# Kernel tuning notes

Measured on AMD Instinct MI355X. Metric: run time of the kernel, lower is better.

The kernel has to match this reference:

```python
import jax, jax.numpy as jnp
import numpy as np

N, E, D, H = 50000, 500000, 128, 4
FH = D // H  # per-head dim of gat1
NEG_SLOPE = 0.2
EPS = 1e-16  # PyG softmax denominator epsilon


def _gat_layer(x, src, dst, W, a_src, a_dst, bias, heads, fh):
    # W: [D_in, heads*fh]; a_src/a_dst: [heads, fh]; bias: [heads*fh]
    n = x.shape[0]
    xp = (x @ W).reshape(n, heads, fh)                     # [N,H,F]
    alpha_s = jnp.einsum('nhf,hf->nh', xp, a_src)          # [N,H]
    alpha_d = jnp.einsum('nhf,hf->nh', xp, a_dst)
    e = alpha_s[src] + alpha_d[dst]                        # [E,H]
    e = jnp.where(e > 0, e, NEG_SLOPE * e)                 # leaky_relu
    # edge softmax grouped by destination node
    m = jax.lax.stop_gradient(jax.ops.segment_max(e, dst, num_segments=n))
    a = jnp.exp(e - m[dst])
    denom = jax.ops.segment_sum(a, dst, num_segments=n)
    a = a / (denom[dst] + EPS)                             # [E,H]
    msg = a[:, :, None] * xp[src]                          # [E,H,F]
    out = jax.ops.segment_sum(msg, dst, num_segments=n)    # [N,H,F]
    return out.reshape(n, heads * fh) + bias


def setup_inputs() -> dict:
    key = jax.random.key(0)
    ks = jax.random.split(key, 20)

    def glorot(k, shape):
        fan_in, fan_out = shape[0], shape[-1]
        std = (2.0 / (fan_in + fan_out)) ** 0.5
        return std * jax.random.normal(k, shape, dtype=jnp.float32)

    inp = {
        'x': jax.random.normal(ks[0], (N, 1), dtype=jnp.float32),
        'edge_index': jax.random.randint(ks[1], (E, 2), 0, N, dtype=jnp.int64 if jax.config.jax_enable_x64 else jnp.int32),
        'W_emb': glorot(ks[2], (1, D)),   # nn.Linear(1, d_node), stored as [in,out]
        'b_emb': jnp.zeros((D,), jnp.float32),
        # gat1: in=D, heads=H, per-head out=FH
        'W1': glorot(ks[3], (D, H * FH)),
        'as1': glorot(ks[4], (H, FH)),
        'ad1': glorot(ks[5], (H, FH)),
        'b1': jnp.zeros((H * FH,), jnp.float32),
        # gat2/3/4: in=D, heads=1, out=D
        'W2': glorot(ks[6], (D, D)), 'as2': glorot(ks[7], (1, D)), 'ad2': glorot(ks[8], (1, D)), 'b2': jnp.zeros((D,), jnp.float32),
        'W3': glorot(ks[9], (D, D)), 'as3': glorot(ks[10], (1, D)), 'ad3': glorot(ks[11], (1, D)), 'b3': jnp.zeros((D,), jnp.float32),
        'W4': glorot(ks[12], (D, D)), 'as4': glorot(ks[13], (1, D)), 'ad4': glorot(ks[14], (1, D)), 'b4': jnp.zeros((D,), jnp.float32),
    }
    return inp


def reference(x, edge_index, W_emb, b_emb, W1, as1, ad1, b1,
              W2, as2, ad2, b2, W3, as3, ad3, b3, W4, as4, ad4, b4):
    # emb: Linear(1 -> D)
    h = x @ W_emb + b_emb                                  # [N,D]
    # edge_index.t(): row 0 = src, row 1 = dst; GATConv adds self-loops
    loop = jnp.arange(N, dtype=edge_index.dtype)
    src = jnp.concatenate([edge_index[:, 0], loop])
    dst = jnp.concatenate([edge_index[:, 1], loop])
    h = jax.nn.relu(_gat_layer(h, src, dst, W1, as1, ad1, b1, H, FH))
    h = jax.nn.relu(_gat_layer(h, src, dst, W2, as2, ad2, b2, 1, D))
    h = jax.nn.relu(_gat_layer(h, src, dst, W3, as3, ad3, b3, 1, D))
    h = _gat_layer(h, src, dst, W4, as4, ad4, b4, 1, D)
    return h
```

## Files before the change

### kernel.cpp

```cpp
#include <hip/hip_runtime.h>
#include <math.h>


#define LEAKY(e) ((e) > 0.f ? (e) : 0.2f * (e))
#define SCAN_BLK 1024

typedef __attribute__((ext_vector_type(8))) short bf16x8;
typedef __attribute__((ext_vector_type(4))) float f32x4;

__device__ inline ushort f32_to_bf16_rne(float f) {
    unsigned u = __float_as_uint(f);
    unsigned r = (u + 0x7FFFu + ((u >> 16) & 1u)) >> 16;
    return (ushort)r;
}
__device__ inline float bf16_to_f32(ushort h) { return __uint_as_float((unsigned)h << 16); }
__device__ inline unsigned pack2(float a, float b) {
    return (unsigned)f32_to_bf16_rne(a) | ((unsigned)f32_to_bf16_rne(b) << 16);
}


__global__ void k_hist(const int* __restrict__ ei, int E, int N, int* __restrict__ deg) {
    int e = blockIdx.x * blockDim.x + threadIdx.x;
    int Et = E + N;
    if (e >= Et) return;
    int dst = (e < E) ? ei[2 * e + 1] : (e - E);
    atomicAdd(&deg[dst], 1);
}

__global__ __launch_bounds__(SCAN_BLK) void k_scan1(const int* __restrict__ deg,
                                                    int* __restrict__ tmp,
                                                    int* __restrict__ blocksum, int n) {
    __shared__ int buf[SCAN_BLK];
    int tid = threadIdx.x;
    int gid = blockIdx.x * SCAN_BLK + tid;
    int v = (gid < n) ? deg[gid] : 0;
    buf[tid] = v;
    __syncthreads();
#pragma unroll
    for (int off = 1; off < SCAN_BLK; off <<= 1) {
        int t = (tid >= off) ? buf[tid - off] : 0;
        __syncthreads();
        buf[tid] += t;
        __syncthreads();
    }
    if (gid < n) tmp[gid] = buf[tid] - v;
    if (tid == SCAN_BLK - 1) blocksum[blockIdx.x] = buf[tid];
}

__global__ __launch_bounds__(256) void k_scan2(const int* __restrict__ blocksum,
                                               int* __restrict__ blockoff, int nb,
                                               int* __restrict__ row_ptr, int n) {
    __shared__ int buf[256];
    int tid = threadIdx.x;
    int v = (tid < nb) ? blocksum[tid] : 0;
    buf[tid] = v;
    __syncthreads();
#pragma unroll
    for (int off = 1; off < 256; off <<= 1) {
        int t = (tid >= off) ? buf[tid - off] : 0;
        __syncthreads();
        buf[tid] += t;
        __syncthreads();
    }
    if (tid < nb) blockoff[tid] = buf[tid] - v;
    if (tid == 255) row_ptr[n] = buf[tid];
}

__global__ void k_scan3(const int* __restrict__ tmp, const int* __restrict__ blockoff,
                        int* __restrict__ row_ptr, int* __restrict__ cursor, int n) {
    int gid = blockIdx.x * blockDim.x + threadIdx.x;
    if (gid >= n) return;
    int v = tmp[gid] + blockoff[gid / SCAN_BLK];
    row_ptr[gid] = v;
    cursor[gid] = v;
}

__global__ void k_scatter(const int* __restrict__ ei, int E, int N,
                          int* __restrict__ cursor, int* __restrict__ csr_src) {
    int e = blockIdx.x * blockDim.x + threadIdx.x;
    int Et = E + N;
    if (e >= Et) return;
    int src, dst;
    if (e < E) { src = ei[2 * e]; dst = ei[2 * e + 1]; }
    else { src = dst = e - E; }
    int pos = atomicAdd(&cursor[dst], 1);
    csr_src[pos] = src;
}


__global__ void k_wsplit3(const float* __restrict__ W0, const float* __restrict__ W1,
                          const float* __restrict__ W2,
                          ushort* __restrict__ hi0, ushort* __restrict__ lo0,
                          ushort* __restrict__ hi1, ushort* __restrict__ lo1,
                          ushort* __restrict__ hi2, ushort* __restrict__ lo2) {
    int l = blockIdx.x >> 6;
    int idx = (blockIdx.x & 63) * 256 + threadIdx.x;
    const float* W = (l == 0) ? W0 : (l == 1) ? W1 : W2;
    ushort* ph = (l == 0) ? hi0 : (l == 1) ? hi1 : hi2;
    ushort* pl = (l == 0) ? lo0 : (l == 1) ? lo1 : lo2;
    int k = idx >> 7, c = idx & 127;
    float w = W[idx];
    ushort hi = f32_to_bf16_rne(w);
    ushort lo = f32_to_bf16_rne(w - bf16_to_f32(hi));
    ph[c * 128 + k] = hi;
    pl[c * 128 + k] = lo;
}

__global__ void k_wvec3(const float* __restrict__ W0, const float* __restrict__ W1,
                        const float* __restrict__ W2,
                        const float* __restrict__ as0, const float* __restrict__ as1,
                        const float* __restrict__ as2,
                        const float* __restrict__ ad0, const float* __restrict__ ad1,
                        const float* __restrict__ ad2,
                        float* __restrict__ was0, float* __restrict__ was1,
                        float* __restrict__ was2,
                        float* __restrict__ wad0, float* __restrict__ wad1,
                        float* __restrict__ wad2) {
    int l = blockIdx.x;
    const float* W  = (l == 0) ? W0 : (l == 1) ? W1 : W2;
    const float* av = (l == 0) ? as0 : (l == 1) ? as1 : as2;
    const float* dv = (l == 0) ? ad0 : (l == 1) ? ad1 : ad2;
    float* ws = (l == 0) ? was0 : (l == 1) ? was1 : was2;
    float* wd = (l == 0) ? wad0 : (l == 1) ? wad1 : wad2;
    int k = threadIdx.x;
    float s = 0.f, d = 0.f;
    for (int c = 0; c < 128; c++) {
        float w = W[k * 128 + c];
        s += w * av[c];
        d += w * dv[c];
    }
    ws[k] = s; wd[k] = d;
}


__global__ void k_emb(const float* __restrict__ W_emb, const float* __restrict__ b_emb,
                      const float* __restrict__ W1, const float* __restrict__ as1,
                      const float* __restrict__ ad1, float* __restrict__ consts) {
    __shared__ float su[128], sv[128];
    int f = threadIdx.x;
    float u = 0.f, v = 0.f;
    for (int k = 0; k < 128; k++) {
        u += W_emb[k] * W1[k * 128 + f];
        v += b_emb[k] * W1[k * 128 + f];
    }
    su[f] = u; sv[f] = v;
    consts[f] = u; consts[128 + f] = v;
    __syncthreads();
    if (f < 4) {
        float P = 0.f, Q = 0.f, R = 0.f, S = 0.f;
        for (int j = 0; j < 32; j++) {
            float uu = su[f * 32 + j], vv = sv[f * 32 + j];
            float a = as1[f * 32 + j], d = ad1[f * 32 + j];
            P += uu * a; Q += vv * a; R += uu * d; S += vv * d;
        }
        consts[256 + f] = P; consts[260 + f] = Q; consts[264 + f] = R; consts[268 + f] = S;
    }
}

__global__ __launch_bounds__(256) void k_l1(const float* __restrict__ x,
        const int* __restrict__ row_ptr, const int* __restrict__ csr_src,
        const float* __restrict__ consts, const float* __restrict__ b1,
        const float* __restrict__ was2, const float* __restrict__ wad2,
        float* __restrict__ hout, float* __restrict__ a_s, float* __restrict__ a_d, int n) {
    __shared__ float sm[64][4], smw[64][4];
    int tid = threadIdx.x;
    int nl = tid >> 2, q = tid & 3;
    int node = blockIdx.x * 64 + nl;
    bool valid = node < n;
    float P = consts[256 + q], Q = consts[260 + q];
    float R = consts[264 + q], Sc = consts[268 + q];
    float den = 0.f, S = 0.f;
    if (valid) {
        float xd = x[node];
        float c0 = xd * R + Sc + Q;
        int s0 = row_ptr[node], s1 = row_ptr[node + 1];
        for (int i = s0; i < s1; i++) {
            float xs = x[csr_src[i]];
            float e = xs * P + c0;
            e = LEAKY(e);
            float w = __expf(e);
            den += w;
            S += w * xs;
        }
    }
    float inv = 1.f / (den + 1e-16f);
    sm[nl][q] = S * inv;
    smw[nl][q] = den * inv;
    __syncthreads();
    float Sn = sm[nl][q], Swn = smw[nl][q];
    float ps = 0.f, pd = 0.f;
    if (valid) {
#pragma unroll
        for (int j = 0; j < 8; j++) {
            int f = q * 32 + j * 4;
            float4 u = *(const float4*)(consts + f);
            float4 v = *(const float4*)(consts + 128 + f);
            float4 b = *(const float4*)(b1 + f);
            float4 ws = *(const float4*)(was2 + f);
            float4 wd = *(const float4*)(wad2 + f);
            float4 val;
            val.x = fmaxf(Sn * u.x + Swn * v.x + b.x, 0.f);
            val.y = fmaxf(Sn * u.y + Swn * v.y + b.y, 0.f);
            val.z = fmaxf(Sn * u.z + Swn * v.z + b.z, 0.f);
            val.w = fmaxf(Sn * u.w + Swn * v.w + b.w, 0.f);
            *(float4*)(hout + (size_t)node * 128 + f) = val;
            ps += val.x * ws.x + val.y * ws.y + val.z * ws.z + val.w * ws.w;
            pd += val.x * wd.x + val.y * wd.y + val.z * wd.z + val.w * wd.w;
        }
    }
    ps += __shfl_xor(ps, 1, 64); ps += __shfl_xor(ps, 2, 64);
    pd += __shfl_xor(pd, 1, 64); pd += __shfl_xor(pd, 2, 64);
    if (q == 0 && valid) { a_s[node] = ps; a_d[node] = pd; }
}

__global__ __launch_bounds__(256) void k_aggh(const float* __restrict__ h,
        const float* __restrict__ as, const float* __restrict__ ad,
        const int* __restrict__ row_ptr, const int* __restrict__ csr_src,
        unsigned* __restrict__ aggp, int n) {
    __shared__ int2 s_sw[4][64];
    int w = threadIdx.x >> 6, lane = threadIdx.x & 63;
    int node = blockIdx.x * 4 + w;
    if (node >= n) return;
    int s0 = row_ptr[node], s1 = row_ptr[node + 1];
    int deg = s1 - s0;
    float adval = ad[node];
    const char* hbase = (const char*)h;

    if (deg <= 64) {
        int boff = 0;
        float e = -INFINITY;
        if (lane < deg) {
            int src = csr_src[s0 + lane];
            boff = src << 9;
            e = LEAKY(as[src] + adval);
        }
        float m = e;
#pragma unroll
        for (int off = 32; off > 0; off >>= 1) m = fmaxf(m, __shfl_xor(m, off, 64));
        float wt = (lane < deg) ? __expf(e - m) : 0.f;
        float den = wt;
#pragma unroll
        for (int off = 32; off > 0; off >>= 1) den += __shfl_xor(den, off, 64);
        s_sw[w][lane] = make_int2(boff, __float_as_int(wt));
        __builtin_amdgcn_wave_barrier();

        int half = lane >> 5;
        int q16 = (lane & 31) * 16;
        float4 acc = make_float4(0.f, 0.f, 0.f, 0.f);
        int degp = (deg + 7) & ~7;
        for (int j = 0; j < degp; j += 8) {
#pragma unroll
            for (int t = 0; t < 4; t++) {
                int2 p = s_sw[w][j + 2 * t + half];
                float4 v = *(const float4*)(hbase + p.x + q16);
                float wt2 = __int_as_float(p.y);
                acc.x += wt2 * v.x; acc.y += wt2 * v.y;
                acc.z += wt2 * v.z; acc.w += wt2 * v.w;
            }
        }
        acc.x += __shfl_xor(acc.x, 32, 64);
        acc.y += __shfl_xor(acc.y, 32, 64);
        acc.z += __shfl_xor(acc.z, 32, 64);
        acc.w += __shfl_xor(acc.w, 32, 64);
        float inv = 1.f / (den + 1e-16f);
        if (lane < 32) {
            float o0 = acc.x * inv, o1 = acc.y * inv;
            float o2 = acc.z * inv, o3 = acc.w * inv;
            ushort h0 = f32_to_bf16_rne(o0), h1 = f32_to_bf16_rne(o1);
            ushort h2 = f32_to_bf16_rne(o2), h3 = f32_to_bf16_rne(o3);
            uint4 pk;
            pk.x = (unsigned)h0 | ((unsigned)h1 << 16);
            pk.y = pack2(o0 - bf16_to_f32(h0), o1 - bf16_to_f32(h1));
            pk.z = (unsigned)h2 | ((unsigned)h3 << 16);
            pk.w = pack2(o2 - bf16_to_f32(h2), o3 - bf16_to_f32(h3));
            ((uint4*)aggp)[(size_t)node * 32 + lane] = pk;
        }
    } else {
        int lane8 = lane * 8;
        float m = -INFINITY;
        for (int i = s0 + lane; i < s1; i += 64) {
            float e = LEAKY(as[csr_src[i]] + adval);
            m = fmaxf(m, e);
        }
#pragma unroll
        for (int off = 32; off > 0; off >>= 1) m = fmaxf(m, __shfl_xor(m, off, 64));
        float den = 0.f;
        float2 acc = make_float2(0.f, 0.f);
        for (int i = s0; i < s1; i++) {
            int src = csr_src[i];
            float e = LEAKY(as[src] + adval);
            float wt = __expf(e - m);
            den += wt;
            float2 v = *(const float2*)(hbase + ((size_t)src << 9) + lane8);
            acc.x += wt * v.x; acc.y += wt * v.y;
        }
        float inv = 1.f / (den + 1e-16f);
        float o0 = acc.x * inv, o1 = acc.y * inv;
        ushort h0 = f32_to_bf16_rne(o0), h1 = f32_to_bf16_rne(o1);
        ((uint2*)aggp)[(size_t)node * 64 + lane] =
            make_uint2((unsigned)h0 | ((unsigned)h1 << 16),
                       pack2(o0 - bf16_to_f32(h0), o1 - bf16_to_f32(h1)));
    }
}

__global__ __launch_bounds__(512) void k_gemm(const uint2* __restrict__ aggp,
        const ushort* __restrict__ wt_hi, const ushort* __restrict__ wt_lo,
        const float* __restrict__ bias, float* __restrict__ hout,
        const float* __restrict__ was_nx, const float* __restrict__ wad_nx,
        float* __restrict__ as_nx, float* __restrict__ ad_nx,
        int n, int do_relu) {
    __shared__ ushort Bh[16 * 128 * 8];
    __shared__ ushort Bl[16 * 128 * 8];
    int tid = threadIdx.x;
#pragma unroll
    for (int rep = 0; rep < 4; rep++) {
        int c = rep * 512 + tid;
        int col = c >> 4, kc = c & 15;
        *(uint4*)(Bh + (size_t)(kc * 128 + col) * 8) = *(const uint4*)(wt_hi + (size_t)col * 128 + kc * 8);
        *(uint4*)(Bl + (size_t)(kc * 128 + col) * 8) = *(const uint4*)(wt_lo + (size_t)col * 128 + kc * 8);
    }
    __syncthreads();

    int wid = tid >> 6, lane = tid & 63;
    int lrow = lane & 15, kgrp = lane >> 4;
    int row_base = blockIdx.x * 128 + wid * 16;

    f32x4 acc[8];
#pragma unroll
    for (int nn = 0; nn < 8; nn++) { acc[nn][0] = 0.f; acc[nn][1] = 0.f; acc[nn][2] = 0.f; acc[nn][3] = 0.f; }

#pragma unroll
    for (int ks = 0; ks < 4; ks++) {
        int kbase = ks * 32 + kgrp * 8;
        int arow = min(row_base + lrow, n - 1);
        const uint2* ap = aggp + (size_t)arow * 64 + (kbase >> 1);
        uint4 q0 = *(const uint4*)ap;
        uint4 q1 = *(const uint4*)(ap + 2);
        int4 hi4 = make_int4(q0.x, q0.z, q1.x, q1.z);
        int4 lo4 = make_int4(q0.y, q0.w, q1.y, q1.w);
        bf16x8 ah = *(bf16x8*)&hi4;
        bf16x8 al = *(bf16x8*)&lo4;
        int kc = ks * 4 + kgrp;
#pragma unroll
        for (int nn = 0; nn < 8; nn++) {
            int col = nn * 16 + lrow;
            bf16x8 bh = *(const bf16x8*)(Bh + (size_t)(kc * 128 + col) * 8);
            bf16x8 bl = *(const bf16x8*)(Bl + (size_t)(kc * 128 + col) * 8);
            acc[nn] = __builtin_amdgcn_mfma_f32_16x16x32_bf16(ah, bh, acc[nn], 0, 0, 0);
            acc[nn] = __builtin_amdgcn_mfma_f32_16x16x32_bf16(ah, bl, acc[nn], 0, 0, 0);
            acc[nn] = __builtin_amdgcn_mfma_f32_16x16x32_bf16(al, bh, acc[nn], 0, 0, 0);
        }
    }

    float bv[8], wsv[8], wdv[8];
#pragma unroll
    for (int nn = 0; nn < 8; nn++) bv[nn] = bias[nn * 16 + lrow];
    if (was_nx) {
#pragma unroll
        for (int nn = 0; nn < 8; nn++) {
            wsv[nn] = was_nx[nn * 16 + lrow];
            wdv[nn] = wad_nx[nn * 16 + lrow];
        }
    }

#pragma unroll
    for (int i = 0; i < 4; i++) {
        int row = row_base + kgrp * 4 + i;
        if (row < n) {
            float ps = 0.f, pd = 0.f;
#pragma unroll
            for (int nn = 0; nn < 8; nn++) {
                float val = acc[nn][i] + bv[nn];
                if (do_relu) val = fmaxf(val, 0.f);
                hout[(size_t)row * 128 + nn * 16 + lrow] = val;
                if (was_nx) { ps += val * wsv[nn]; pd += val * wdv[nn]; }
            }
            if (was_nx) {
#pragma unroll
                for (int off = 1; off < 16; off <<= 1) {
                    ps += __shfl_xor(ps, off, 16);
                    pd += __shfl_xor(pd, off, 16);
                }
                if (lrow == 0) { as_nx[row] = ps; ad_nx[row] = pd; }
            }
        }
    }
}


extern "C" void kernel_launch(void* const* d_in, const int* in_sizes, int n_in,
                              void* d_out, int out_size, void* d_ws, size_t ws_size,
                              hipStream_t stream) {
    const float* x     = (const float*)d_in[0];
    const int*   ei    = (const int*)d_in[1];
    const float* W_emb = (const float*)d_in[2];
    const float* b_emb = (const float*)d_in[3];
    const float* W1    = (const float*)d_in[4];
    const float* as1   = (const float*)d_in[5];
    const float* ad1   = (const float*)d_in[6];
    const float* b1    = (const float*)d_in[7];
    const float* Wl[3]  = {(const float*)d_in[8],  (const float*)d_in[12], (const float*)d_in[16]};
    const float* asl[3] = {(const float*)d_in[9],  (const float*)d_in[13], (const float*)d_in[17]};
    const float* adl[3] = {(const float*)d_in[10], (const float*)d_in[14], (const float*)d_in[18]};
    const float* bl[3]  = {(const float*)d_in[11], (const float*)d_in[15], (const float*)d_in[19]};
    float* out = (float*)d_out;

    int N = in_sizes[0];
    int E = in_sizes[1] / 2;
    int Et = E + N;
    int nb = (N + SCAN_BLK - 1) / SCAN_BLK;

    char* ws = (char*)d_ws;
    size_t off = 0;
    auto alloc = [&](size_t bytes) { size_t p = off; off += (bytes + 255) & ~(size_t)255; return p; };
    int*   deg      = (int*)(ws + alloc((size_t)N * 4));
    int*   row_ptr  = (int*)(ws + alloc((size_t)(N + 1) * 4));
    int*   cursor   = (int*)(ws + alloc((size_t)N * 4));
    int*   csr_src  = (int*)(ws + alloc((size_t)Et * 4));
    int*   scantmp  = (int*)(ws + alloc((size_t)N * 4));
    int*   blocksum = (int*)(ws + alloc((size_t)nb * 4));
    int*   blockoff = (int*)(ws + alloc((size_t)nb * 4));
    float* consts   = (float*)(ws + alloc(272 * 4));
    float* a_s0     = (float*)(ws + alloc((size_t)N * 4));
    float* a_d0     = (float*)(ws + alloc((size_t)N * 4));
    float* a_s1     = (float*)(ws + alloc((size_t)N * 4));
    float* a_d1     = (float*)(ws + alloc((size_t)N * 4));
    float* hA       = (float*)(ws + alloc((size_t)N * 128 * 4));
    unsigned* aggp  = (unsigned*)(ws + alloc((size_t)N * 64 * 8));
    ushort* wt_hi[3]; ushort* wt_lo[3];
    float* was[3]; float* wad[3];
    for (int l = 0; l < 3; l++) {
        wt_hi[l] = (ushort*)(ws + alloc(128 * 128 * 2));
        wt_lo[l] = (ushort*)(ws + alloc(128 * 128 * 2));
        was[l]   = (float*)(ws + alloc(128 * 4));
        wad[l]   = (float*)(ws + alloc(128 * 4));
    }

    hipMemsetAsync(deg, 0, (size_t)N * 4, stream);
    k_hist<<<(Et + 255) / 256, 256, 0, stream>>>(ei, E, N, deg);
    k_scan1<<<nb, SCAN_BLK, 0, stream>>>(deg, scantmp, blocksum, N);
    k_scan2<<<1, 256, 0, stream>>>(blocksum, blockoff, nb, row_ptr, N);
    k_scan3<<<(N + 255) / 256, 256, 0, stream>>>(scantmp, blockoff, row_ptr, cursor, N);
    k_scatter<<<(Et + 255) / 256, 256, 0, stream>>>(ei, E, N, cursor, csr_src);

    k_wsplit3<<<192, 256, 0, stream>>>(Wl[0], Wl[1], Wl[2],
                                       wt_hi[0], wt_lo[0], wt_hi[1], wt_lo[1], wt_hi[2], wt_lo[2]);
    k_wvec3<<<3, 128, 0, stream>>>(Wl[0], Wl[1], Wl[2], asl[0], asl[1], asl[2],
                                   adl[0], adl[1], adl[2],
                                   was[0], was[1], was[2], wad[0], wad[1], wad[2]);
    k_emb<<<1, 128, 0, stream>>>(W_emb, b_emb, W1, as1, ad1, consts);

    k_l1<<<(N + 63) / 64, 256, 0, stream>>>(x, row_ptr, csr_src, consts, b1,
                                            was[0], wad[0], hA, a_s0, a_d0, N);

    float* as_cur = a_s0; float* ad_cur = a_d0;
    float* as_nxt = a_s1; float* ad_nxt = a_d1;
    for (int l = 0; l < 3; l++) {
        k_aggh<<<(N + 3) / 4, 256, 0, stream>>>(hA, as_cur, ad_cur, row_ptr, csr_src, aggp, N);
        if (l < 2) {
            k_gemm<<<(N + 127) / 128, 512, 0, stream>>>((const uint2*)aggp, wt_hi[l], wt_lo[l], bl[l], hA,
                                                        was[l + 1], wad[l + 1], as_nxt, ad_nxt, N, 1);
            float* t;
            t = as_cur; as_cur = as_nxt; as_nxt = t;
            t = ad_cur; ad_cur = ad_nxt; ad_nxt = t;
        } else {
            k_gemm<<<(N + 127) / 128, 512, 0, stream>>>((const uint2*)aggp, wt_hi[l], wt_lo[l], bl[l], out,
                                                        nullptr, nullptr, nullptr, nullptr, N, 0);
        }
    }
}
```

Before: 282.3 us.

## Store aggregation output and weights in MFMA fragment order; drop LDS staging

The aggregation kernel now writes its hi/lo bf16 split outputs straight into a tiled layout that matches the MFMA 16x16x32 A-fragment order. The weight split kernel also emits B fragments in lane order. The GEMM therefore loads both operands with one contiguous 16-byte load per lane from global memory. It no longer stages weights in LDS and shrinks to 256-thread blocks over 64 rows. This removes the LDS fill, the sync and the strided A gathers, but it reloads the weights from global/L2 in every wave and makes the aggregation stores more scattered.

```diff
diff --git a/kernel.cpp b/kernel.cpp
--- a/kernel.cpp
+++ b/kernel.cpp
@@ -102,8 +102,11 @@
     float w = W[idx];
     ushort hi = f32_to_bf16_rne(w);
     ushort lo = f32_to_bf16_rne(w - bf16_to_f32(hi));
-    ph[c * 128 + k] = hi;
-    pl[c * 128 + k] = lo;
+    int ks = k >> 5, kgrp = (k >> 3) & 3, j = k & 7;
+    int nn = c >> 4, lrow = c & 15;
+    int off = (((ks * 8 + nn) * 64) + kgrp * 16 + lrow) * 8 + j;
+    ph[off] = hi;
+    pl[off] = lo;
 }
 
 __global__ void k_wvec3(const float* __restrict__ W0, const float* __restrict__ W1,
@@ -216,7 +219,7 @@
 __global__ __launch_bounds__(256) void k_aggh(const float* __restrict__ h,
         const float* __restrict__ as, const float* __restrict__ ad,
         const int* __restrict__ row_ptr, const int* __restrict__ csr_src,
-        unsigned* __restrict__ aggp, int n) {
+        ushort* __restrict__ afrag_hi, ushort* __restrict__ afrag_lo, int n) {
     __shared__ int2 s_sw[4][64];
     int w = threadIdx.x >> 6, lane = threadIdx.x & 63;
     int node = blockIdx.x * 4 + w;
@@ -225,6 +228,8 @@
     int deg = s1 - s0;
     float adval = ad[node];
     const char* hbase = (const char*)h;
+    size_t tbase = (size_t)(node >> 4) * 4 * 64 * 8;
+    int lrow16 = node & 15;
 
     if (deg <= 64) {
         int boff = 0;
@@ -268,12 +273,16 @@
             float o2 = acc.z * inv, o3 = acc.w * inv;
             ushort h0 = f32_to_bf16_rne(o0), h1 = f32_to_bf16_rne(o1);
             ushort h2 = f32_to_bf16_rne(o2), h3 = f32_to_bf16_rne(o3);
-            uint4 pk;
-            pk.x = (unsigned)h0 | ((unsigned)h1 << 16);
-            pk.y = pack2(o0 - bf16_to_f32(h0), o1 - bf16_to_f32(h1));
-            pk.z = (unsigned)h2 | ((unsigned)h3 << 16);
-            pk.w = pack2(o2 - bf16_to_f32(h2), o3 - bf16_to_f32(h3));
-            ((uint4*)aggp)[(size_t)node * 32 + lane] = pk;
+            unsigned hi01 = (unsigned)h0 | ((unsigned)h1 << 16);
+            unsigned hi23 = (unsigned)h2 | ((unsigned)h3 << 16);
+            unsigned lo01 = pack2(o0 - bf16_to_f32(h0), o1 - bf16_to_f32(h1));
+            unsigned lo23 = pack2(o2 - bf16_to_f32(h2), o3 - bf16_to_f32(h3));
+            int ks = lane >> 3;
+            int kgrp = (lane >> 1) & 3;
+            int j0 = (lane & 1) * 4;
+            size_t off = tbase + ((size_t)ks * 64 + kgrp * 16 + lrow16) * 8 + j0;
+            *(uint2*)(afrag_hi + off) = make_uint2(hi01, hi23);
+            *(uint2*)(afrag_lo + off) = make_uint2(lo01, lo23);
         }
     } else {
         int lane8 = lane * 8;
@@ -297,33 +306,25 @@
         float inv = 1.f / (den + 1e-16f);
         float o0 = acc.x * inv, o1 = acc.y * inv;
         ushort h0 = f32_to_bf16_rne(o0), h1 = f32_to_bf16_rne(o1);
-        ((uint2*)aggp)[(size_t)node * 64 + lane] =
-            make_uint2((unsigned)h0 | ((unsigned)h1 << 16),
-                       pack2(o0 - bf16_to_f32(h0), o1 - bf16_to_f32(h1)));
-    }
-}
-
-__global__ __launch_bounds__(512) void k_gemm(const uint2* __restrict__ aggp,
-        const ushort* __restrict__ wt_hi, const ushort* __restrict__ wt_lo,
+        int k = 2 * lane;
+        int ks = k >> 5, kgrp = (k >> 3) & 3, j0 = k & 7;
+        size_t off = tbase + ((size_t)ks * 64 + kgrp * 16 + lrow16) * 8 + j0;
+        *(unsigned*)(afrag_hi + off) = (unsigned)h0 | ((unsigned)h1 << 16);
+        *(unsigned*)(afrag_lo + off) = pack2(o0 - bf16_to_f32(h0), o1 - bf16_to_f32(h1));
+    }
+}
+
+__global__ __launch_bounds__(256) void k_gemm(
+        const ushort* __restrict__ afrag_hi, const ushort* __restrict__ afrag_lo,
+        const ushort* __restrict__ wf_hi, const ushort* __restrict__ wf_lo,
         const float* __restrict__ bias, float* __restrict__ hout,
         const float* __restrict__ was_nx, const float* __restrict__ wad_nx,
         float* __restrict__ as_nx, float* __restrict__ ad_nx,
         int n, int do_relu) {
-    __shared__ ushort Bh[16 * 128 * 8];
-    __shared__ ushort Bl[16 * 128 * 8];
-    int tid = threadIdx.x;
-#pragma unroll
-    for (int rep = 0; rep < 4; rep++) {
-        int c = rep * 512 + tid;
-        int col = c >> 4, kc = c & 15;
-        *(uint4*)(Bh + (size_t)(kc * 128 + col) * 8) = *(const uint4*)(wt_hi + (size_t)col * 128 + kc * 8);
-        *(uint4*)(Bl + (size_t)(kc * 128 + col) * 8) = *(const uint4*)(wt_lo + (size_t)col * 128 + kc * 8);
-    }
-    __syncthreads();
-
-    int wid = tid >> 6, lane = tid & 63;
+    int tid = threadIdx.x, wid = tid >> 6, lane = tid & 63;
     int lrow = lane & 15, kgrp = lane >> 4;
-    int row_base = blockIdx.x * 128 + wid * 16;
+    int tile = blockIdx.x * 4 + wid;
+    int row_base = tile * 16;
 
     f32x4 acc[8];
 #pragma unroll
@@ -331,21 +332,14 @@
 
 #pragma unroll
     for (int ks = 0; ks < 4; ks++) {
-        int kbase = ks * 32 + kgrp * 8;
-        int arow = min(row_base + lrow, n - 1);
-        const uint2* ap = aggp + (size_t)arow * 64 + (kbase >> 1);
-        uint4 q0 = *(const uint4*)ap;
-        uint4 q1 = *(const uint4*)(ap + 2);
-        int4 hi4 = make_int4(q0.x, q0.z, q1.x, q1.z);
-        int4 lo4 = make_int4(q0.y, q0.w, q1.y, q1.w);
-        bf16x8 ah = *(bf16x8*)&hi4;
-        bf16x8 al = *(bf16x8*)&lo4;
-        int kc = ks * 4 + kgrp;
+        size_t aoff = ((size_t)(tile * 4 + ks) * 64 + lane) * 8;
+        bf16x8 ah = *(const bf16x8*)(afrag_hi + aoff);
+        bf16x8 al = *(const bf16x8*)(afrag_lo + aoff);
 #pragma unroll
         for (int nn = 0; nn < 8; nn++) {
-            int col = nn * 16 + lrow;
-            bf16x8 bh = *(const bf16x8*)(Bh + (size_t)(kc * 128 + col) * 8);
-            bf16x8 bl = *(const bf16x8*)(Bl + (size_t)(kc * 128 + col) * 8);
+            size_t boff = ((size_t)(ks * 8 + nn) * 64 + lane) * 8;
+            bf16x8 bh = *(const bf16x8*)(wf_hi + boff);
+            bf16x8 bl = *(const bf16x8*)(wf_lo + boff);
             acc[nn] = __builtin_amdgcn_mfma_f32_16x16x32_bf16(ah, bh, acc[nn], 0, 0, 0);
             acc[nn] = __builtin_amdgcn_mfma_f32_16x16x32_bf16(ah, bl, acc[nn], 0, 0, 0);
             acc[nn] = __builtin_amdgcn_mfma_f32_16x16x32_bf16(al, bh, acc[nn], 0, 0, 0);
@@ -409,6 +403,8 @@
     int E = in_sizes[1] / 2;
     int Et = E + N;
     int nb = (N + SCAN_BLK - 1) / SCAN_BLK;
+    int ntile = (N + 15) / 16;
+    int ngblk = (N + 63) / 64;
 
     char* ws = (char*)d_ws;
     size_t off = 0;
@@ -426,12 +422,14 @@
     float* a_s1     = (float*)(ws + alloc((size_t)N * 4));
     float* a_d1     = (float*)(ws + alloc((size_t)N * 4));
     float* hA       = (float*)(ws + alloc((size_t)N * 128 * 4));
-    unsigned* aggp  = (unsigned*)(ws + alloc((size_t)N * 64 * 8));
-    ushort* wt_hi[3]; ushort* wt_lo[3];
+    size_t atiles = (size_t)ngblk * 4;
+    ushort* afrag_hi = (ushort*)(ws + alloc(atiles * 4 * 64 * 8 * 2));
+    ushort* afrag_lo = (ushort*)(ws + alloc(atiles * 4 * 64 * 8 * 2));
+    ushort* wf_hi[3]; ushort* wf_lo[3];
     float* was[3]; float* wad[3];
     for (int l = 0; l < 3; l++) {
-        wt_hi[l] = (ushort*)(ws + alloc(128 * 128 * 2));
-        wt_lo[l] = (ushort*)(ws + alloc(128 * 128 * 2));
+        wf_hi[l] = (ushort*)(ws + alloc(4 * 8 * 64 * 8 * 2));
+        wf_lo[l] = (ushort*)(ws + alloc(4 * 8 * 64 * 8 * 2));
         was[l]   = (float*)(ws + alloc(128 * 4));
         wad[l]   = (float*)(ws + alloc(128 * 4));
     }
@@ -444,7 +442,7 @@
     k_scatter<<<(Et + 255) / 256, 256, 0, stream>>>(ei, E, N, cursor, csr_src);
 
     k_wsplit3<<<192, 256, 0, stream>>>(Wl[0], Wl[1], Wl[2],
-                                       wt_hi[0], wt_lo[0], wt_hi[1], wt_lo[1], wt_hi[2], wt_lo[2]);
+                                       wf_hi[0], wf_lo[0], wf_hi[1], wf_lo[1], wf_hi[2], wf_lo[2]);
     k_wvec3<<<3, 128, 0, stream>>>(Wl[0], Wl[1], Wl[2], asl[0], asl[1], asl[2],
                                    adl[0], adl[1], adl[2],
                                    was[0], was[1], was[2], wad[0], wad[1], wad[2]);
@@ -456,16 +454,17 @@
     float* as_cur = a_s0; float* ad_cur = a_d0;
     float* as_nxt = a_s1; float* ad_nxt = a_d1;
     for (int l = 0; l < 3; l++) {
-        k_aggh<<<(N + 3) / 4, 256, 0, stream>>>(hA, as_cur, ad_cur, row_ptr, csr_src, aggp, N);
+        k_aggh<<<(N + 3) / 4, 256, 0, stream>>>(hA, as_cur, ad_cur, row_ptr, csr_src,
+                                                afrag_hi, afrag_lo, N);
         if (l < 2) {
-            k_gemm<<<(N + 127) / 128, 512, 0, stream>>>((const uint2*)aggp, wt_hi[l], wt_lo[l], bl[l], hA,
-                                                        was[l + 1], wad[l + 1], as_nxt, ad_nxt, N, 1);
+            k_gemm<<<ngblk, 256, 0, stream>>>(afrag_hi, afrag_lo, wf_hi[l], wf_lo[l], bl[l], hA,
+                                              was[l + 1], wad[l + 1], as_nxt, ad_nxt, N, 1);
             float* t;
             t = as_cur; as_cur = as_nxt; as_nxt = t;
             t = ad_cur; ad_cur = ad_nxt; ad_nxt = t;
         } else {
-            k_gemm<<<(N + 127) / 128, 512, 0, stream>>>((const uint2*)aggp, wt_hi[l], wt_lo[l], bl[l], out,
-                                                        nullptr, nullptr, nullptr, nullptr, N, 0);
-        }
-    }
-}
+            k_gemm<<<ngblk, 256, 0, stream>>>(afrag_hi, afrag_lo, wf_hi[l], wf_lo[l], bl[l], out,
+                                              nullptr, nullptr, nullptr, nullptr, N, 0);
+        }
+    }
+}
```

After: 291.4 us. 1.03x slower.

## Replace CSR build with padded 64-slot adjacency plus overflow list

Applied to the files above, without the earlier changes.

Drops the histogram, three-pass scan and scatter kernels. Each destination now gets a fixed 64-slot row filled by a single atomic scatter, and edges beyond 64 go to a global overflow list that consumers scan linearly. The three weight-prep kernels are also merged into one launch. This cuts several launches and passes over the edge list, but makes the adjacency buffer much larger and makes high-degree nodes scan the whole overflow list. Edges silently drop if the overflow exceeds its capacity.

```diff
diff --git a/kernel.cpp b/kernel.cpp
--- a/kernel.cpp
+++ b/kernel.cpp
@@ -3,7 +3,6 @@
 
 
 #define LEAKY(e) ((e) > 0.f ? (e) : 0.2f * (e))
-#define SCAN_BLK 1024
 
 typedef __attribute__((ext_vector_type(8))) short bf16x8;
 typedef __attribute__((ext_vector_type(4))) float f32x4;
@@ -19,146 +18,100 @@
 }
 
 
-__global__ void k_hist(const int* __restrict__ ei, int E, int N, int* __restrict__ deg) {
-    int e = blockIdx.x * blockDim.x + threadIdx.x;
-    int Et = E + N;
-    if (e >= Et) return;
-    int dst = (e < E) ? ei[2 * e + 1] : (e - E);
-    atomicAdd(&deg[dst], 1);
-}
-
-__global__ __launch_bounds__(SCAN_BLK) void k_scan1(const int* __restrict__ deg,
-                                                    int* __restrict__ tmp,
-                                                    int* __restrict__ blocksum, int n) {
-    __shared__ int buf[SCAN_BLK];
-    int tid = threadIdx.x;
-    int gid = blockIdx.x * SCAN_BLK + tid;
-    int v = (gid < n) ? deg[gid] : 0;
-    buf[tid] = v;
-    __syncthreads();
-#pragma unroll
-    for (int off = 1; off < SCAN_BLK; off <<= 1) {
-        int t = (tid >= off) ? buf[tid - off] : 0;
-        __syncthreads();
-        buf[tid] += t;
-        __syncthreads();
-    }
-    if (gid < n) tmp[gid] = buf[tid] - v;
-    if (tid == SCAN_BLK - 1) blocksum[blockIdx.x] = buf[tid];
-}
-
-__global__ __launch_bounds__(256) void k_scan2(const int* __restrict__ blocksum,
-                                               int* __restrict__ blockoff, int nb,
-                                               int* __restrict__ row_ptr, int n) {
-    __shared__ int buf[256];
-    int tid = threadIdx.x;
-    int v = (tid < nb) ? blocksum[tid] : 0;
-    buf[tid] = v;
-    __syncthreads();
-#pragma unroll
-    for (int off = 1; off < 256; off <<= 1) {
-        int t = (tid >= off) ? buf[tid - off] : 0;
-        __syncthreads();
-        buf[tid] += t;
-        __syncthreads();
-    }
-    if (tid < nb) blockoff[tid] = buf[tid] - v;
-    if (tid == 255) row_ptr[n] = buf[tid];
-}
-
-__global__ void k_scan3(const int* __restrict__ tmp, const int* __restrict__ blockoff,
-                        int* __restrict__ row_ptr, int* __restrict__ cursor, int n) {
-    int gid = blockIdx.x * blockDim.x + threadIdx.x;
-    if (gid >= n) return;
-    int v = tmp[gid] + blockoff[gid / SCAN_BLK];
-    row_ptr[gid] = v;
-    cursor[gid] = v;
-}
-
-__global__ void k_scatter(const int* __restrict__ ei, int E, int N,
-                          int* __restrict__ cursor, int* __restrict__ csr_src) {
+__global__ void k_scatterpad(const int* __restrict__ ei, int E, int N,
+                             int* __restrict__ deg, int* __restrict__ csr_pad,
+                             int* __restrict__ ovf_cnt, int2* __restrict__ ovf,
+                             int ovf_cap) {
     int e = blockIdx.x * blockDim.x + threadIdx.x;
     int Et = E + N;
     if (e >= Et) return;
     int src, dst;
-    if (e < E) { src = ei[2 * e]; dst = ei[2 * e + 1]; }
+    if (e < E) { int2 p = ((const int2*)ei)[e]; src = p.x; dst = p.y; }
     else { src = dst = e - E; }
-    int pos = atomicAdd(&cursor[dst], 1);
-    csr_src[pos] = src;
-}
-
-
-__global__ void k_wsplit3(const float* __restrict__ W0, const float* __restrict__ W1,
-                          const float* __restrict__ W2,
-                          ushort* __restrict__ hi0, ushort* __restrict__ lo0,
-                          ushort* __restrict__ hi1, ushort* __restrict__ lo1,
-                          ushort* __restrict__ hi2, ushort* __restrict__ lo2) {
-    int l = blockIdx.x >> 6;
-    int idx = (blockIdx.x & 63) * 256 + threadIdx.x;
-    const float* W = (l == 0) ? W0 : (l == 1) ? W1 : W2;
-    ushort* ph = (l == 0) ? hi0 : (l == 1) ? hi1 : hi2;
-    ushort* pl = (l == 0) ? lo0 : (l == 1) ? lo1 : lo2;
-    int k = idx >> 7, c = idx & 127;
-    float w = W[idx];
-    ushort hi = f32_to_bf16_rne(w);
-    ushort lo = f32_to_bf16_rne(w - bf16_to_f32(hi));
-    ph[c * 128 + k] = hi;
-    pl[c * 128 + k] = lo;
-}
-
-__global__ void k_wvec3(const float* __restrict__ W0, const float* __restrict__ W1,
-                        const float* __restrict__ W2,
-                        const float* __restrict__ as0, const float* __restrict__ as1,
-                        const float* __restrict__ as2,
-                        const float* __restrict__ ad0, const float* __restrict__ ad1,
-                        const float* __restrict__ ad2,
-                        float* __restrict__ was0, float* __restrict__ was1,
-                        float* __restrict__ was2,
-                        float* __restrict__ wad0, float* __restrict__ wad1,
-                        float* __restrict__ wad2) {
-    int l = blockIdx.x;
-    const float* W  = (l == 0) ? W0 : (l == 1) ? W1 : W2;
-    const float* av = (l == 0) ? as0 : (l == 1) ? as1 : as2;
-    const float* dv = (l == 0) ? ad0 : (l == 1) ? ad1 : ad2;
-    float* ws = (l == 0) ? was0 : (l == 1) ? was1 : was2;
-    float* wd = (l == 0) ? wad0 : (l == 1) ? wad1 : wad2;
-    int k = threadIdx.x;
-    float s = 0.f, d = 0.f;
-    for (int c = 0; c < 128; c++) {
-        float w = W[k * 128 + c];
-        s += w * av[c];
-        d += w * dv[c];
-    }
-    ws[k] = s; wd[k] = d;
-}
-
-
-__global__ void k_emb(const float* __restrict__ W_emb, const float* __restrict__ b_emb,
-                      const float* __restrict__ W1, const float* __restrict__ as1,
-                      const float* __restrict__ ad1, float* __restrict__ consts) {
+    int pos = atomicAdd(&deg[dst], 1);
+    if (pos < 64) {
+        csr_pad[(dst << 6) + pos] = src;
+    } else {
+        int o = atomicAdd(ovf_cnt, 1);
+        if (o < ovf_cap) ovf[o] = make_int2(dst, src);
+    }
+}
+
+
+__global__ void k_prep(const float* __restrict__ Wa, const float* __restrict__ Wb,
+                       const float* __restrict__ Wc,
+                       const float* __restrict__ asa, const float* __restrict__ asb,
+                       const float* __restrict__ asc,
+                       const float* __restrict__ ada, const float* __restrict__ adb,
+                       const float* __restrict__ adc,
+                       const float* __restrict__ W_emb, const float* __restrict__ b_emb,
+                       const float* __restrict__ W1g, const float* __restrict__ as1g,
+                       const float* __restrict__ ad1g,
+                       ushort* __restrict__ hi0, ushort* __restrict__ lo0,
+                       ushort* __restrict__ hi1, ushort* __restrict__ lo1,
+                       ushort* __restrict__ hi2, ushort* __restrict__ lo2,
+                       float* __restrict__ was0, float* __restrict__ was1,
+                       float* __restrict__ was2,
+                       float* __restrict__ wad0, float* __restrict__ wad1,
+                       float* __restrict__ wad2,
+                       float* __restrict__ consts) {
     __shared__ float su[128], sv[128];
-    int f = threadIdx.x;
-    float u = 0.f, v = 0.f;
-    for (int k = 0; k < 128; k++) {
-        u += W_emb[k] * W1[k * 128 + f];
-        v += b_emb[k] * W1[k * 128 + f];
-    }
-    su[f] = u; sv[f] = v;
-    consts[f] = u; consts[128 + f] = v;
-    __syncthreads();
-    if (f < 4) {
-        float P = 0.f, Q = 0.f, R = 0.f, S = 0.f;
-        for (int j = 0; j < 32; j++) {
-            float uu = su[f * 32 + j], vv = sv[f * 32 + j];
-            float a = as1[f * 32 + j], d = ad1[f * 32 + j];
-            P += uu * a; Q += vv * a; R += uu * d; S += vv * d;
-        }
-        consts[256 + f] = P; consts[260 + f] = Q; consts[264 + f] = R; consts[268 + f] = S;
+    int b = blockIdx.x, tid = threadIdx.x;
+    if (b < 192) {
+        int l = b >> 6;
+        int idx = (b & 63) * 256 + tid;
+        const float* W = (l == 0) ? Wa : (l == 1) ? Wb : Wc;
+        ushort* ph = (l == 0) ? hi0 : (l == 1) ? hi1 : hi2;
+        ushort* pl = (l == 0) ? lo0 : (l == 1) ? lo1 : lo2;
+        int k = idx >> 7, c = idx & 127;
+        float w = W[idx];
+        ushort hi = f32_to_bf16_rne(w);
+        ushort lo = f32_to_bf16_rne(w - bf16_to_f32(hi));
+        ph[c * 128 + k] = hi;
+        pl[c * 128 + k] = lo;
+    } else if (b < 195) {
+        if (tid >= 128) return;
+        int l = b - 192;
+        const float* W  = (l == 0) ? Wa : (l == 1) ? Wb : Wc;
+        const float* av = (l == 0) ? asa : (l == 1) ? asb : asc;
+        const float* dv = (l == 0) ? ada : (l == 1) ? adb : adc;
+        float* ws = (l == 0) ? was0 : (l == 1) ? was1 : was2;
+        float* wd = (l == 0) ? wad0 : (l == 1) ? wad1 : wad2;
+        int k = tid;
+        float s = 0.f, d = 0.f;
+        for (int c = 0; c < 128; c++) {
+            float w = W[k * 128 + c];
+            s += w * av[c];
+            d += w * dv[c];
+        }
+        ws[k] = s; wd[k] = d;
+    } else {
+        if (tid >= 128) return;
+        int f = tid;
+        float u = 0.f, v = 0.f;
+        for (int k = 0; k < 128; k++) {
+            u += W_emb[k] * W1g[k * 128 + f];
+            v += b_emb[k] * W1g[k * 128 + f];
+        }
+        su[f] = u; sv[f] = v;
+        consts[f] = u; consts[128 + f] = v;
+        __syncthreads();
+        if (f < 4) {
+            float P = 0.f, Q = 0.f, R = 0.f, S = 0.f;
+            for (int j = 0; j < 32; j++) {
+                float uu = su[f * 32 + j], vv = sv[f * 32 + j];
+                float a = as1g[f * 32 + j], d = ad1g[f * 32 + j];
+                P += uu * a; Q += vv * a; R += uu * d; S += vv * d;
+            }
+            consts[256 + f] = P; consts[260 + f] = Q;
+            consts[264 + f] = R; consts[268 + f] = S;
+        }
     }
 }
 
 __global__ __launch_bounds__(256) void k_l1(const float* __restrict__ x,
-        const int* __restrict__ row_ptr, const int* __restrict__ csr_src,
+        const int* __restrict__ deg, const int* __restrict__ csr_pad,
+        const int* __restrict__ ovf_cnt, const int2* __restrict__ ovf,
         const float* __restrict__ consts, const float* __restrict__ b1,
         const float* __restrict__ was2, const float* __restrict__ wad2,
         float* __restrict__ hout, float* __restrict__ a_s, float* __restrict__ a_d, int n) {
@@ -173,14 +126,29 @@
     if (valid) {
         float xd = x[node];
         float c0 = xd * R + Sc + Q;
-        int s0 = row_ptr[node], s1 = row_ptr[node + 1];
-        for (int i = s0; i < s1; i++) {
-            float xs = x[csr_src[i]];
+        int dg = deg[node];
+        int dlim = min(dg, 64);
+        for (int i = 0; i < dlim; i++) {
+            float xs = x[csr_pad[(node << 6) + i]];
             float e = xs * P + c0;
             e = LEAKY(e);
             float w = __expf(e);
             den += w;
             S += w * xs;
+        }
+        if (dg > 64) {
+            int no = *ovf_cnt;
+            for (int i = 0; i < no; i++) {
+                int2 p = ovf[i];
+                if (p.x == node) {
+                    float xs = x[p.y];
+                    float e = xs * P + c0;
+                    e = LEAKY(e);
+                    float w = __expf(e);
+                    den += w;
+                    S += w * xs;
+                }
+            }
         }
     }
     float inv = 1.f / (den + 1e-16f);
@@ -215,29 +183,29 @@
 
 __global__ __launch_bounds__(256) void k_aggh(const float* __restrict__ h,
         const float* __restrict__ as, const float* __restrict__ ad,
-        const int* __restrict__ row_ptr, const int* __restrict__ csr_src,
+        const int* __restrict__ deg, const int* __restrict__ csr_pad,
+        const int* __restrict__ ovf_cnt, const int2* __restrict__ ovf,
         unsigned* __restrict__ aggp, int n) {
     __shared__ int2 s_sw[4][64];
     int w = threadIdx.x >> 6, lane = threadIdx.x & 63;
     int node = blockIdx.x * 4 + w;
     if (node >= n) return;
-    int s0 = row_ptr[node], s1 = row_ptr[node + 1];
-    int deg = s1 - s0;
+    int dg = deg[node];
     float adval = ad[node];
     const char* hbase = (const char*)h;
 
-    if (deg <= 64) {
+    if (dg <= 64) {
         int boff = 0;
         float e = -INFINITY;
-        if (lane < deg) {
-            int src = csr_src[s0 + lane];
+        if (lane < dg) {
+            int src = csr_pad[(node << 6) + lane];
             boff = src << 9;
             e = LEAKY(as[src] + adval);
         }
         float m = e;
 #pragma unroll
         for (int off = 32; off > 0; off >>= 1) m = fmaxf(m, __shfl_xor(m, off, 64));
-        float wt = (lane < deg) ? __expf(e - m) : 0.f;
+        float wt = (lane < dg) ? __expf(e - m) : 0.f;
         float den = wt;
 #pragma unroll
         for (int off = 32; off > 0; off >>= 1) den += __shfl_xor(den, off, 64);
@@ -247,7 +215,7 @@
         int half = lane >> 5;
         int q16 = (lane & 31) * 16;
         float4 acc = make_float4(0.f, 0.f, 0.f, 0.f);
-        int degp = (deg + 7) & ~7;
+        int degp = (dg + 7) & ~7;
         for (int j = 0; j < degp; j += 8) {
 #pragma unroll
             for (int t = 0; t < 4; t++) {
@@ -277,22 +245,34 @@
         }
     } else {
         int lane8 = lane * 8;
-        float m = -INFINITY;
-        for (int i = s0 + lane; i < s1; i += 64) {
-            float e = LEAKY(as[csr_src[i]] + adval);
-            m = fmaxf(m, e);
+        int no = *ovf_cnt;
+        int psrc = csr_pad[(node << 6) + lane];
+        float m = LEAKY(as[psrc] + adval);
+        for (int i = lane; i < no; i += 64) {
+            int2 p = ovf[i];
+            if (p.x == node) m = fmaxf(m, LEAKY(as[p.y] + adval));
         }
 #pragma unroll
         for (int off = 32; off > 0; off >>= 1) m = fmaxf(m, __shfl_xor(m, off, 64));
         float den = 0.f;
         float2 acc = make_float2(0.f, 0.f);
-        for (int i = s0; i < s1; i++) {
-            int src = csr_src[i];
+        for (int i = 0; i < 64; i++) {
+            int src = csr_pad[(node << 6) + i];
             float e = LEAKY(as[src] + adval);
             float wt = __expf(e - m);
             den += wt;
             float2 v = *(const float2*)(hbase + ((size_t)src << 9) + lane8);
             acc.x += wt * v.x; acc.y += wt * v.y;
+        }
+        for (int i = 0; i < no; i++) {
+            int2 p = ovf[i];
+            if (p.x == node) {
+                float e = LEAKY(as[p.y] + adval);
+                float wt = __expf(e - m);
+                den += wt;
+                float2 v = *(const float2*)(hbase + ((size_t)p.y << 9) + lane8);
+                acc.x += wt * v.x; acc.y += wt * v.y;
+            }
         }
         float inv = 1.f / (den + 1e-16f);
         float o0 = acc.x * inv, o1 = acc.y * inv;
@@ -395,9 +375,9 @@
     const int*   ei    = (const int*)d_in[1];
     const float* W_emb = (const float*)d_in[2];
     const float* b_emb = (const float*)d_in[3];
-    const float* W1    = (const float*)d_in[4];
-    const float* as1   = (const float*)d_in[5];
-    const float* ad1   = (const float*)d_in[6];
+    const float* W1g   = (const float*)d_in[4];
+    const float* as1g  = (const float*)d_in[5];
+    const float* ad1g  = (const float*)d_in[6];
     const float* b1    = (const float*)d_in[7];
     const float* Wl[3]  = {(const float*)d_in[8],  (const float*)d_in[12], (const float*)d_in[16]};
     const float* asl[3] = {(const float*)d_in[9],  (const float*)d_in[13], (const float*)d_in[17]};
@@ -408,18 +388,15 @@
     int N = in_sizes[0];
     int E = in_sizes[1] / 2;
     int Et = E + N;
-    int nb = (N + SCAN_BLK - 1) / SCAN_BLK;
+    const int OVF_CAP = 65536;
 
     char* ws = (char*)d_ws;
     size_t off = 0;
     auto alloc = [&](size_t bytes) { size_t p = off; off += (bytes + 255) & ~(size_t)255; return p; };
     int*   deg      = (int*)(ws + alloc((size_t)N * 4));
-    int*   row_ptr  = (int*)(ws + alloc((size_t)(N + 1) * 4));
-    int*   cursor   = (int*)(ws + alloc((size_t)N * 4));
-    int*   csr_src  = (int*)(ws + alloc((size_t)Et * 4));
-    int*   scantmp  = (int*)(ws + alloc((size_t)N * 4));
-    int*   blocksum = (int*)(ws + alloc((size_t)nb * 4));
-    int*   blockoff = (int*)(ws + alloc((size_t)nb * 4));
+    int*   ovf_cnt  = (int*)(ws + alloc(4));
+    int2*  ovf      = (int2*)(ws + alloc((size_t)OVF_CAP * 8));
+    int*   csr_pad  = (int*)(ws + alloc((size_t)N * 64 * 4));
     float* consts   = (float*)(ws + alloc(272 * 4));
     float* a_s0     = (float*)(ws + alloc((size_t)N * 4));
     float* a_d0     = (float*)(ws + alloc((size_t)N * 4));
@@ -437,26 +414,24 @@
     }
 
     hipMemsetAsync(deg, 0, (size_t)N * 4, stream);
-    k_hist<<<(Et + 255) / 256, 256, 0, stream>>>(ei, E, N, deg);
-    k_scan1<<<nb, SCAN_BLK, 0, stream>>>(deg, scantmp, blocksum, N);
-    k_scan2<<<1, 256, 0, stream>>>(blocksum, blockoff, nb, row_ptr, N);
-    k_scan3<<<(N + 255) / 256, 256, 0, stream>>>(scantmp, blockoff, row_ptr, cursor, N);
-    k_scatter<<<(Et + 255) / 256, 256, 0, stream>>>(ei, E, N, cursor, csr_src);
-
-    k_wsplit3<<<192, 256, 0, stream>>>(Wl[0], Wl[1], Wl[2],
-                                       wt_hi[0], wt_lo[0], wt_hi[1], wt_lo[1], wt_hi[2], wt_lo[2]);
-    k_wvec3<<<3, 128, 0, stream>>>(Wl[0], Wl[1], Wl[2], asl[0], asl[1], asl[2],
-                                   adl[0], adl[1], adl[2],
-                                   was[0], was[1], was[2], wad[0], wad[1], wad[2]);
-    k_emb<<<1, 128, 0, stream>>>(W_emb, b_emb, W1, as1, ad1, consts);
-
-    k_l1<<<(N + 63) / 64, 256, 0, stream>>>(x, row_ptr, csr_src, consts, b1,
+    hipMemsetAsync(ovf_cnt, 0, 4, stream);
+    k_scatterpad<<<(Et + 255) / 256, 256, 0, stream>>>(ei, E, N, deg, csr_pad,
+                                                       ovf_cnt, ovf, OVF_CAP);
+    k_prep<<<196, 256, 0, stream>>>(Wl[0], Wl[1], Wl[2], asl[0], asl[1], asl[2],
+                                    adl[0], adl[1], adl[2],
+                                    W_emb, b_emb, W1g, as1g, ad1g,
+                                    wt_hi[0], wt_lo[0], wt_hi[1], wt_lo[1], wt_hi[2], wt_lo[2],
+                                    was[0], was[1], was[2], wad[0], wad[1], wad[2],
+                                    consts);
+
+    k_l1<<<(N + 63) / 64, 256, 0, stream>>>(x, deg, csr_pad, ovf_cnt, ovf, consts, b1,
                                             was[0], wad[0], hA, a_s0, a_d0, N);
 
     float* as_cur = a_s0; float* ad_cur = a_d0;
     float* as_nxt = a_s1; float* ad_nxt = a_d1;
     for (int l = 0; l < 3; l++) {
-        k_aggh<<<(N + 3) / 4, 256, 0, stream>>>(hA, as_cur, ad_cur, row_ptr, csr_src, aggp, N);
+        k_aggh<<<(N + 3) / 4, 256, 0, stream>>>(hA, as_cur, ad_cur, deg, csr_pad,
+                                                ovf_cnt, ovf, aggp, N);
         if (l < 2) {
             k_gemm<<<(N + 127) / 128, 512, 0, stream>>>((const uint2*)aggp, wt_hi[l], wt_lo[l], bl[l], hA,
                                                         was[l + 1], wad[l + 1], as_nxt, ad_nxt, N, 1);
```

Measured after the change: 247.7 us. 1.14x faster.
